# Optimization experiments

Hardware: AMD Instinct MI355X
Metric: run time of the kernel (lower is better)

## Reference

```python
import jax, jax.numpy as jnp
import numpy as np

H, D = 20, 64  # heads, head_dim (hidden_size = 1280)


def setup_inputs() -> dict:
    key = jax.random.key(0)
    ks = jax.random.split(key, 10)
    B, S, HID, CROSS, T_TXT, T_IP = 8, 4096, 1280, 2048, 77, 4
    w = lambda k, shp: jax.random.normal(k, shp, dtype=jnp.float32) * 0.02
    return {
        "hidden_states": jax.random.normal(ks[0], (B, S, HID), dtype=jnp.float32),
        "encoder_hidden_states": jax.random.normal(ks[1], (B, T_TXT, CROSS), dtype=jnp.float32),
        "ip_hidden_states": jax.random.normal(ks[2], (B, T_IP, CROSS), dtype=jnp.float32),
        "Wq": w(ks[3], (HID, HID)),
        "Wk": w(ks[4], (CROSS, HID)),
        "Wv": w(ks[5], (CROSS, HID)),
        "Wk_ip": w(ks[6], (CROSS, HID)),
        "Wv_ip": w(ks[7], (CROSS, HID)),
        "Wo": w(ks[8], (HID, HID)),
        "bo": jnp.zeros((HID,), dtype=jnp.float32),
    }


def _attend(q, kv_in, Wk, Wv):
    # q: [B,S,H,D]; kv_in: [B,T,cross]
    B, T = kv_in.shape[0], kv_in.shape[1]
    k = (kv_in @ Wk).reshape(B, T, H, D)
    v = (kv_in @ Wv).reshape(B, T, H, D)
    scale = 1.0 / jnp.sqrt(jnp.asarray(D, q.dtype))
    scores = jnp.einsum("bqhd,bkhd->bhqk", q, k) * scale
    probs = jax.nn.softmax(scores, axis=-1)
    out = jnp.einsum("bhqk,bkhd->bqhd", probs, v)
    return out.reshape(B, q.shape[1], H * D)


def reference(hidden_states, encoder_hidden_states, ip_hidden_states,
              Wq, Wk, Wv, Wk_ip, Wv_ip, Wo, bo):
    B, S, _ = hidden_states.shape
    q = (hidden_states @ Wq).reshape(B, S, H, D)
    # text cross-attention branch
    out = _attend(q, encoder_hidden_states, Wk, Wv)
    # IP-adapter branch (single adapter, scale=1.0, no mask)
    ip_scale = 1.0
    out = out + ip_scale * _attend(q, ip_hidden_states, Wk_ip, Wv_ip)
    # output projection (dropout is identity at inference)
    return out @ Wo + bo
```

## Files before the change

kernel.cpp:

```cpp
#include <hip/hip_runtime.h>

using u16 = unsigned short;
using u32 = unsigned int;
typedef __bf16 bf16x8 __attribute__((ext_vector_type(8)));
typedef float f32x4 __attribute__((ext_vector_type(4)));
typedef float f32x16 __attribute__((ext_vector_type(16)));

__device__ __forceinline__ u16 f2bf(float f) {
  u32 u = __float_as_uint(f);
  u += 0x7FFFu + ((u >> 16) & 1u);
  return (u16)(u >> 16);
}

__device__ __forceinline__ u32 cvtpk(float a, float b) {
  u32 r;
  asm("v_cvt_pk_bf16_f32 %0, %1, %2" : "=v"(r) : "v"(a), "v"(b));
  return r;
}

__device__ __forceinline__ void gload16(const u16* g, u16* l) {
  __builtin_amdgcn_global_load_lds((const __attribute__((address_space(1))) void*)g,
                                   (__attribute__((address_space(3))) void*)l, 16, 0, 0);
}

__global__ void prep_all(const float* __restrict__ enc, const float* __restrict__ ip,
                         u16* __restrict__ a_all,
                         const float* __restrict__ Wk, const float* __restrict__ Wv,
                         const float* __restrict__ Wkip, const float* __restrict__ Wvip,
                         u16* __restrict__ kvw,
                         const float* __restrict__ Wq, const float* __restrict__ Wo,
                         u16* __restrict__ wq_t, u16* __restrict__ wo_t) {
  const int bid = blockIdx.x;
  const int tid = threadIdx.x;
  if (bid < 1536) {
    const int i = bid * 256 + tid;
    const int row = i >> 9;
    const int c4 = i & 511;
    ushort4 o = {0, 0, 0, 0};
    const float4* src = nullptr;
    if (row < 616) src = (const float4*)enc + (size_t)row * 512 + c4;
    else if (row >= 640 && row < 672) src = (const float4*)ip + (size_t)(row - 640) * 512 + c4;
    if (src) {
      const float4 v = *src;
      o.x = f2bf(v.x); o.y = f2bf(v.y); o.z = f2bf(v.z); o.w = f2bf(v.w);
    }
    ((ushort4*)a_all)[i] = o;
    return;
  }
  __shared__ float tile[32][33];
  const int x = tid & 31, y = tid >> 5;
  const float* in;
  u16* out;
  int K, N, n0, k0;
  if (bid < 11776) {
    const int f = bid - 1536;
    const int z = f / 2560, rem = f % 2560;
    in = (z == 0) ? Wk : (z == 1) ? Wv : (z == 2) ? Wkip : Wvip;
    out = kvw + (size_t)z * 1280 * 2048;
    K = 2048; N = 1280;
    n0 = (rem % 40) << 5; k0 = (rem / 40) << 5;
  } else {
    const int f = bid - 11776;
    const int z = f / 1600, rem = f % 1600;
    in = z ? Wo : Wq;
    out = z ? wo_t : wq_t;
    K = 1280; N = 1280;
    n0 = (rem % 40) << 5; k0 = (rem / 40) << 5;
  }
#pragma unroll
  for (int i = 0; i < 32; i += 8)
    tile[y + i][x] = in[(size_t)(k0 + y + i) * N + n0 + x];
  __syncthreads();
#pragma unroll
  for (int i = 0; i < 32; i += 8)
    out[(size_t)(n0 + y + i) * K + k0 + x] = f2bf(tile[x][y + i]);
}

#define MFMA16(a, b, c) __builtin_amdgcn_mfma_f32_16x16x32_bf16(a, b, c, 0, 0, 0)
#define MFMA32(a, b, c) __builtin_amdgcn_mfma_f32_32x32x16_bf16(a, b, c, 0, 0, 0)

__global__ __launch_bounds__(512, 2) void gemm256kv(
    const u16* __restrict__ A, const u16* __restrict__ Bt, u16* __restrict__ Cb,
    const float* __restrict__ convSrc, u16* __restrict__ convDst,
    int M, int N, int K) {
  const int tid = threadIdx.x;

  if (blockIdx.x >= 60) {
    const float4* src = (const float4*)convSrc;
    ushort4* dst = (ushort4*)convDst;
    const long base = (long)(blockIdx.x - 60) * 4096 + tid;
#pragma unroll
    for (int k = 0; k < 8; ++k) {
      const float4 v = src[base + k * 512];
      ushort4 o;
      o.x = f2bf(v.x); o.y = f2bf(v.y); o.z = f2bf(v.z); o.w = f2bf(v.w);
      dst[base + k * 512] = o;
    }
    return;
  }

  __shared__ __align__(16) u16 smem[65536];
  u16* As = smem;
  u16* Bs = smem + 32768;

  const int w = tid >> 6, lane = tid & 63;
  const int lo = lane & 15, hi = lane >> 4;
  const int wm = w >> 2, wn = w & 3;

  const int nbn = N >> 8;
  const int wg = blockIdx.x;
  const int bm = wg / nbn, bn = wg % nbn;
  const int m0 = bm << 8, n0 = bn << 8;
  const int NT = K >> 6;

  const int sr = lane >> 3;
  const int sc8 = ((lane & 7) ^ sr) << 3;
  const u16* pA[2];
  const u16* pB[2];
#pragma unroll
  for (int i = 0; i < 2; ++i) {
    const int rr = (i * 8 + w) * 8 + sr;
    pA[i] = A + (size_t)(m0 + rr) * K + sc8;
    pB[i] = Bt + (size_t)(n0 + rr) * K + sc8;
  }
  const int ch0 = w * 512, ch1 = (8 + w) * 512;

#define STAGE_A(h, tt)                                                     \
  {                                                                        \
    const int ttc = ((tt) < NT) ? (tt) : (NT - 1);                         \
    u16* d = As + ((((tt)&1) * 2 + (h)) << 13);                            \
    const size_t off = (size_t)(h)*128 * K + (size_t)ttc * 64;             \
    gload16(pA[0] + off, d + ch0);                                         \
    gload16(pA[1] + off, d + ch1);                                         \
  }
#define STAGE_B(h, tt)                                                     \
  {                                                                        \
    const int ttc = ((tt) < NT) ? (tt) : (NT - 1);                         \
    u16* d = Bs + ((((tt)&1) * 2 + (h)) << 13);                            \
    const size_t off = (size_t)(h)*128 * K + (size_t)ttc * 64;             \
    gload16(pB[0] + off, d + ch0);                                         \
    gload16(pB[1] + off, d + ch1);                                         \
  }

  const int low0 = (lo << 7) | ((hi ^ (lo & 7)) << 4);
  const int low1 = (lo << 7) | (((4 | hi) ^ (lo & 7)) << 4);

  f32x4 acc[8][4];
#pragma unroll
  for (int i = 0; i < 8; ++i)
#pragma unroll
    for (int j = 0; j < 4; ++j) acc[i][j] = (f32x4){0.f, 0.f, 0.f, 0.f};

  STAGE_B(0, 0); STAGE_B(1, 0);
  STAGE_A(0, 0); STAGE_A(1, 0);
  STAGE_B(0, 1); STAGE_B(1, 1);

  const char* aSm = (const char*)As;
  const char* bSm = (const char*)Bs;

  for (int t = 0; t < NT; ++t) {
    const int p = t & 1;
    const int aBase = (p * 2 + wm) << 14;
    const int bBase = ((p * 2 + (wn >> 1)) << 14) + ((wn & 1) << 13);

    asm volatile("s_waitcnt vmcnt(4)" ::: "memory");
    asm volatile("s_barrier" ::: "memory");

    bf16x8 a0[4][2], a1[4][2], b0[2][2], b1[2][2];
#pragma unroll
    for (int mf = 0; mf < 4; ++mf) {
      a0[mf][0] = *(const bf16x8*)(aSm + aBase + (mf << 11) + low0);
      a0[mf][1] = *(const bf16x8*)(aSm + aBase + (mf << 11) + low1);
    }
#pragma unroll
    for (int nf = 0; nf < 2; ++nf) {
      b0[nf][0] = *(const bf16x8*)(bSm + bBase + (nf << 11) + low0);
      b0[nf][1] = *(const bf16x8*)(bSm + bBase + (nf << 11) + low1);
    }
    STAGE_A(0, t + 1);
    __builtin_amdgcn_s_setprio(1);
#pragma unroll
    for (int mf = 0; mf < 4; ++mf)
#pragma unroll
      for (int nf = 0; nf < 2; ++nf) {
        acc[mf][nf] = MFMA16(a0[mf][0], b0[nf][0], acc[mf][nf]);
        acc[mf][nf] = MFMA16(a0[mf][1], b0[nf][1], acc[mf][nf]);
      }
    __builtin_amdgcn_s_setprio(0);

#pragma unroll
    for (int nf = 0; nf < 2; ++nf) {
      b1[nf][0] = *(const bf16x8*)(bSm + bBase + (1 << 12) + (nf << 11) + low0);
      b1[nf][1] = *(const bf16x8*)(bSm + bBase + (1 << 12) + (nf << 11) + low1);
    }
    STAGE_A(1, t + 1);
    __builtin_amdgcn_s_setprio(1);
#pragma unroll
    for (int mf = 0; mf < 4; ++mf)
#pragma unroll
      for (int nf = 0; nf < 2; ++nf) {
        acc[mf][2 + nf] = MFMA16(a0[mf][0], b1[nf][0], acc[mf][2 + nf]);
        acc[mf][2 + nf] = MFMA16(a0[mf][1], b1[nf][1], acc[mf][2 + nf]);
      }
    __builtin_amdgcn_s_setprio(0);
    asm volatile("s_barrier" ::: "memory");

#pragma unroll
    for (int mf = 0; mf < 4; ++mf) {
      a1[mf][0] = *(const bf16x8*)(aSm + aBase + (1 << 13) + (mf << 11) + low0);
      a1[mf][1] = *(const bf16x8*)(aSm + aBase + (1 << 13) + (mf << 11) + low1);
    }
    STAGE_B(0, t + 2);
    __builtin_amdgcn_s_setprio(1);
#pragma unroll
    for (int mf = 0; mf < 4; ++mf)
#pragma unroll
      for (int nf = 0; nf < 2; ++nf) {
        acc[4 + mf][nf] = MFMA16(a1[mf][0], b0[nf][0], acc[4 + mf][nf]);
        acc[4 + mf][nf] = MFMA16(a1[mf][1], b0[nf][1], acc[4 + mf][nf]);
      }
    __builtin_amdgcn_s_setprio(0);

    STAGE_B(1, t + 2);
    __builtin_amdgcn_s_setprio(1);
#pragma unroll
    for (int mf = 0; mf < 4; ++mf)
#pragma unroll
      for (int nf = 0; nf < 2; ++nf) {
        acc[4 + mf][2 + nf] = MFMA16(a1[mf][0], b1[nf][0], acc[4 + mf][2 + nf]);
        acc[4 + mf][2 + nf] = MFMA16(a1[mf][1], b1[nf][1], acc[4 + mf][2 + nf]);
      }
    __builtin_amdgcn_s_setprio(0);
  }

#pragma unroll
  for (int g = 0; g < 2; ++g)
#pragma unroll
    for (int mf = 0; mf < 4; ++mf)
#pragma unroll
      for (int ng = 0; ng < 2; ++ng)
#pragma unroll
        for (int nfi = 0; nfi < 2; ++nfi) {
          const f32x4 v = acc[g * 4 + mf][ng * 2 + nfi];
          const int row0 = m0 + wm * 128 + g * 64 + mf * 16 + hi * 4;
          const int col = n0 + wn * 64 + ng * 32 + nfi * 16 + lo;
#pragma unroll
          for (int r = 0; r < 4; ++r)
            Cb[(size_t)(row0 + r) * N + col] = f2bf(v[r]);
        }
#undef STAGE_A
#undef STAGE_B
}

template <int MODE>
__global__ __launch_bounds__(256, 2) void gemm128(
    const u16* __restrict__ A, const u16* __restrict__ Bt,
    u16* __restrict__ Cb, float* __restrict__ Cf, const float* __restrict__ bias,
    const u16* __restrict__ kvcP, const u16* __restrict__ vtP,
    int M, int N, int K) {
  __shared__ __align__(16) u16 smem[32768];
  const int tid = threadIdx.x;
  const int w = tid >> 6, lane = tid & 63;
  const int lo = lane & 15, hi = lane >> 4;
  const int wm = w >> 1, wn = w & 1;

  const int nbn = N >> 7;
  int wg = blockIdx.x;
  {
    const int nwg = gridDim.x;
    const int q = nwg >> 3, r = nwg & 7;
    const int xcd = wg & 7, l = wg >> 3;
    wg = (xcd < r ? xcd * (q + 1) : r * (q + 1) + (xcd - r) * q) + l;
  }
  const int bm = wg / nbn, bn = wg % nbn;
  const int m0 = bm << 7, n0 = bn << 7;
  const int NT = K >> 6;

  const int sr = lane >> 3;
  const int sc8 = ((lane & 7) ^ sr) << 3;
  const u16 *pA[4], *pB[4];
#pragma unroll
  for (int j = 0; j < 4; ++j) {
    const int rr = (w + j * 4) * 8 + sr;
    pA[j] = A + (size_t)(m0 + rr) * K + sc8;
    pB[j] = Bt + (size_t)(n0 + rr) * K + sc8;
  }

#define STG128(tt)                                                         \
  {                                                                        \
    const int ttc = ((tt) < NT) ? (tt) : (NT - 1);                         \
    const int bofs = (((tt)&1) << 13);          \
    const size_t off = (size_t)ttc * 64;                                   \
    _Pragma("unroll") for (int j = 0; j < 4; ++j) {                        \
      gload16(pA[j] + off, smem + bofs + (w + j * 4) * 512);               \
      gload16(pB[j] + off, smem + 16384 + bofs + (w + j * 4) * 512);       \
    }                                                                      \
  }

  const int low0 = (lo << 7) | ((hi ^ (lo & 7)) << 4);
  const int low1 = (lo << 7) | (((4 | hi) ^ (lo & 7)) << 4);
  const char* aSm = (const char*)smem;
  const char* bSm = (const char*)(smem + 16384);

  f32x4 acc[4][4];
#pragma unroll
  for (int i = 0; i < 4; ++i)
#pragma unroll
    for (int j = 0; j < 4; ++j) acc[i][j] = (f32x4){0.f, 0.f, 0.f, 0.f};

  STG128(0); STG128(1);

  for (int t = 0; t < NT; ++t) {
    const int aBase = ((t & 1) << 14) + (wm << 13);
    const int bBase = ((t & 1) << 14) + (wn << 13);

    asm volatile("s_waitcnt vmcnt(8)" ::: "memory");
    asm volatile("s_barrier" ::: "memory");

    bf16x8 a[4][2], b[4][2];
#pragma unroll
    for (int mf = 0; mf < 4; ++mf) {
      a[mf][0] = *(const bf16x8*)(aSm + aBase + (mf << 11) + low0);
      a[mf][1] = *(const bf16x8*)(aSm + aBase + (mf << 11) + low1);
    }
#pragma unroll
    for (int nf = 0; nf < 4; ++nf) {
      b[nf][0] = *(const bf16x8*)(bSm + bBase + (nf << 11) + low0);
      b[nf][1] = *(const bf16x8*)(bSm + bBase + (nf << 11) + low1);
    }
    asm volatile("s_waitcnt lgkmcnt(0)" ::: "memory");
    __builtin_amdgcn_sched_barrier(0);
    asm volatile("s_barrier" ::: "memory");
    STG128(t + 2);
    __builtin_amdgcn_s_setprio(1);
#pragma unroll
    for (int mf = 0; mf < 4; ++mf)
#pragma unroll
      for (int nf = 0; nf < 4; ++nf) {
        acc[mf][nf] = MFMA16(a[mf][0], b[nf][0], acc[mf][nf]);
        acc[mf][nf] = MFMA16(a[mf][1], b[nf][1], acc[mf][nf]);
      }
    __builtin_amdgcn_s_setprio(0);
  }

  if (MODE == 1) {
#pragma unroll
    for (int mf = 0; mf < 4; ++mf)
#pragma unroll
      for (int nf = 0; nf < 4; ++nf) {
        const int row0 = m0 + wm * 64 + mf * 16 + hi * 4;
        const int col = n0 + wn * 64 + nf * 16 + lo;
        const float bb = bias[col];
#pragma unroll
        for (int r = 0; r < 4; ++r)
          Cf[(size_t)(row0 + r) * N + col] = acc[mf][nf][r] + bb;
      }
  } else {
    const int l31 = lane & 31, hi5 = lane >> 5;
    const int h = bn * 2 + wn;
    const int b = m0 >> 12;

    bf16x8 kreg[3][4];
#pragma unroll
    for (int kf = 0; kf < 3; ++kf) {
      const int key = kf * 32 + l31;
      const u16* kp;
      if (key < 77) kp = kvcP + (size_t)(b * 77 + key) * 5120 + h * 64 + hi5 * 8;
      else if (key >= 80 && key < 84)
        kp = kvcP + (size_t)(640 + b * 4 + key - 80) * 5120 + 2560 + h * 64 + hi5 * 8;
      else kp = kvcP + h * 64 + hi5 * 8;
#pragma unroll
      for (int dc = 0; dc < 4; ++dc) kreg[kf][dc] = *(const bf16x8*)(kp + dc * 16);
    }

    asm volatile("s_waitcnt vmcnt(0)" ::: "memory");
    __builtin_amdgcn_s_barrier();

    u16* qlds = smem + w * 4224;
#pragma unroll
    for (int mf = 0; mf < 4; ++mf)
#pragma unroll
      for (int nf = 0; nf < 4; ++nf) {
        const f32x4 v = acc[mf][nf];
        const int qrow = mf * 16 + hi * 4;
        const int d = nf * 16 + lo;
#pragma unroll
        for (int r = 0; r < 4; ++r) qlds[(qrow + r) * 66 + d] = f2bf(v[r]);
      }

    bf16x8 qf0[4], qf1[4];
#pragma unroll
    for (int dc = 0; dc < 4; ++dc) {
      qf0[dc] = *(const bf16x8*)&qlds[(l31)*66 + dc * 16 + hi5 * 8];
      qf1[dc] = *(const bf16x8*)&qlds[(32 + l31) * 66 + dc * 16 + hi5 * 8];
    }

    f32x16 s0[3], s1[3];
#pragma unroll
    for (int kf = 0; kf < 3; ++kf)
#pragma unroll
      for (int r = 0; r < 16; ++r) { s0[kf][r] = 0.f; s1[kf][r] = 0.f; }

#pragma unroll
    for (int kf = 0; kf < 3; ++kf)
#pragma unroll
      for (int dc = 0; dc < 4; ++dc) {
        s0[kf] = MFMA32(kreg[kf][dc], qf0[dc], s0[kf]);
        s1[kf] = MFMA32(kreg[kf][dc], qf1[dc], s1[kf]);
      }

    float st0 = 0.f, si0 = 0.f, st1 = 0.f, si1 = 0.f;
#pragma unroll
    for (int kf = 0; kf < 3; ++kf)
#pragma unroll
      for (int r = 0; r < 16; ++r) {
        const int krem = (r & 3) + 8 * (r >> 2);
        const int k = kf * 32 + krem + 4 * hi5;
        const bool vtx = k < 77;
        const bool vip = (k >= 80) & (k < 84);
        const float e0 = (vtx | vip) ? __expf(s0[kf][r] * 0.125f) : 0.f;
        const float e1 = (vtx | vip) ? __expf(s1[kf][r] * 0.125f) : 0.f;
        s0[kf][r] = e0; s1[kf][r] = e1;
        st0 += vtx ? e0 : 0.f; si0 += vip ? e0 : 0.f;
        st1 += vtx ? e1 : 0.f; si1 += vip ? e1 : 0.f;
      }
    st0 += __shfl_xor(st0, 32); si0 += __shfl_xor(si0, 32);
    st1 += __shfl_xor(st1, 32); si1 += __shfl_xor(si1, 32);
    const float rt0 = __fdividef(1.f, st0), ri0 = __fdividef(1.f, si0);
    const float rt1 = __fdividef(1.f, st1), ri1 = __fdividef(1.f, si1);
#pragma unroll
    for (int kf = 0; kf < 3; ++kf)
#pragma unroll
      for (int r = 0; r < 16; ++r) {
        const int krem = (r & 3) + 8 * (r >> 2);
        const int k = kf * 32 + krem + 4 * hi5;
        const bool vip = (k >= 80) & (k < 84);
        s0[kf][r] *= vip ? ri0 : rt0;
        s1[kf][r] *= vip ? ri1 : rt1;
      }

    const u16* vbase = vtP + ((size_t)(b * 20 + h) * 64) * 96 + hi5 * 8;
    const int rowB = m0 + wm * 64;

#define PV_STORE(sA, qoff)                                                  \
    {                                                                       \
      f32x16 pacc[2];                                                       \
      _Pragma("unroll") for (int nf = 0; nf < 2; ++nf)                      \
      _Pragma("unroll") for (int r = 0; r < 16; ++r) pacc[nf][r] = 0.f;     \
      _Pragma("unroll") for (int ks = 0; ks < 6; ++ks) {                    \
        const int kf = ks >> 1;                                             \
        const int rb = (ks & 1) * 8;                                        \
        const u32 lo01 = cvtpk(sA[kf][rb + 0], sA[kf][rb + 1]);             \
        const u32 lo23 = cvtpk(sA[kf][rb + 2], sA[kf][rb + 3]);             \
        const u32 hi01 = cvtpk(sA[kf][rb + 4], sA[kf][rb + 5]);             \
        const u32 hi23 = cvtpk(sA[kf][rb + 6], sA[kf][rb + 7]);             \
        const u32 plo01 = __shfl_xor(lo01, 32);                             \
        const u32 plo23 = __shfl_xor(lo23, 32);                             \
        const u32 phi01 = __shfl_xor(hi01, 32);                             \
        const u32 phi23 = __shfl_xor(hi23, 32);                             \
        union { u32 u[4]; bf16x8 v; } pu;                                   \
        pu.u[0] = hi5 ? phi01 : lo01;                                       \
        pu.u[1] = hi5 ? phi23 : lo23;                                       \
        pu.u[2] = hi5 ? hi01 : plo01;                                       \
        pu.u[3] = hi5 ? hi23 : plo23;                                       \
        _Pragma("unroll") for (int nf = 0; nf < 2; ++nf) {                  \
          const bf16x8 vb = *(const bf16x8*)(vbase +                        \
              (size_t)(nf * 32 + l31) * 96 + ks * 16);                      \
          pacc[nf] = MFMA32(pu.v, vb, pacc[nf]);                            \
        }                                                                   \
      }                                                                     \
      _Pragma("unroll") for (int nf = 0; nf < 2; ++nf)                      \
      _Pragma("unroll") for (int r = 0; r < 16; ++r) {                      \
        const int row = rowB + (qoff) + (r & 3) + 8 * (r >> 2) + 4 * hi5;   \
        Cb[(size_t)row * 1280 + h * 64 + nf * 32 + l31] = f2bf(pacc[nf][r]);\
      }                                                                     \
    }

    PV_STORE(s0, 0)
    PV_STORE(s1, 32)
#undef PV_STORE
  }
#undef STG128
}

__global__ __launch_bounds__(256) void build_vt(const u16* __restrict__ kvc,
                                                u16* __restrict__ vt) {
  __shared__ u16 Ls[96][72];
  const int tid = threadIdx.x;
  const int h = blockIdx.x % 20, b = blockIdx.x / 20;
  for (int idx = tid; idx < 96 * 8; idx += 256) {
    const int row = idx >> 3, c8 = (idx & 7) << 3;
    uint4 val = make_uint4(0, 0, 0, 0);
    if (row < 77)
      val = *(const uint4*)(kvc + (size_t)(b * 77 + row) * 5120 + 1280 + h * 64 + c8);
    else if (row >= 80 && row < 84)
      val = *(const uint4*)(kvc + (size_t)(640 + b * 4 + row - 80) * 5120 + 3840 + h * 64 + c8);
    *(uint4*)&Ls[row][c8] = val;
  }
  __syncthreads();
  u16* dst = vt + (size_t)blockIdx.x * 64 * 96;
  for (int idx = tid; idx < 768; idx += 256) {
    const int d = idx / 12, c = (idx % 12) * 8;
    u16 tmp[8];
#pragma unroll
    for (int j = 0; j < 8; ++j) tmp[j] = Ls[c + j][d];
    *(uint4*)(dst + d * 96 + c) = *(const uint4*)tmp;
  }
}

extern "C" void kernel_launch(void* const* d_in, const int* in_sizes, int n_in,
                              void* d_out, int out_size, void* d_ws, size_t ws_size,
                              hipStream_t stream) {
  (void)in_sizes; (void)n_in; (void)out_size; (void)ws_size;
  const float* hs   = (const float*)d_in[0];
  const float* enc  = (const float*)d_in[1];
  const float* ip   = (const float*)d_in[2];
  const float* Wq   = (const float*)d_in[3];
  const float* Wk   = (const float*)d_in[4];
  const float* Wv   = (const float*)d_in[5];
  const float* Wkip = (const float*)d_in[6];
  const float* Wvip = (const float*)d_in[7];
  const float* Wo   = (const float*)d_in[8];
  const float* bo   = (const float*)d_in[9];
  float* out = (float*)d_out;

  u16* wq_t  = (u16*)d_out;
  u16* hs_bf = (u16*)d_out + 41943040;

  char* ws = (char*)d_ws;
  u16* kvc   = (u16*)(ws);
  u16* wo_t  = (u16*)(ws + 15728640);
  u16* vt    = (u16*)(ws + 19005440);
  u16* attn  = (u16*)(ws + 20971520);
  u16* kvw   = (u16*)(ws + 20971520 + 3276800);
  u16* a_all = (u16*)(ws + 20971520 + 24248320);

  prep_all<<<14976, 256, 0, stream>>>(enc, ip, a_all, Wk, Wv, Wkip, Wvip, kvw,
                                      Wq, Wo, wq_t, wo_t);

  gemm256kv<<<2620, 512, 0, stream>>>(a_all, kvw, kvc, hs, hs_bf, 768, 5120, 2048);
  build_vt<<<160, 256, 0, stream>>>(kvc, vt);

  gemm128<2><<<2560, 256, 0, stream>>>(hs_bf, wq_t, attn, nullptr, nullptr,
                                       kvc, vt, 32768, 1280, 1280);

  gemm128<1><<<2560, 256, 0, stream>>>(attn, wo_t, nullptr, out, bo,
                                       nullptr, nullptr, 32768, 1280, 1280);
}
```

Measured before the change: 347.3 us.

## Split fused Q-projection attention into separate GEMM and attention kernels

Q projection GEMM now writes bf16 Q to global memory, and a new standalone attn3 kernel computes the text+IP attention from it instead of doing it in the GEMM epilogue. The hidden_states fp32-to-bf16 conversion is moved from the KV GEMM launch into the prep kernel. This frees the GEMM epilogue of the register and LDS pressure of attention, but adds a full write and re-read of Q through HBM plus an extra launch.

```diff
diff --git a/kernel.cpp b/kernel.cpp
--- a/kernel.cpp
+++ b/kernel.cpp
@@ -29,9 +29,23 @@
                          const float* __restrict__ Wkip, const float* __restrict__ Wvip,
                          u16* __restrict__ kvw,
                          const float* __restrict__ Wq, const float* __restrict__ Wo,
-                         u16* __restrict__ wq_t, u16* __restrict__ wo_t) {
+                         u16* __restrict__ wq_t, u16* __restrict__ wo_t,
+                         const float* __restrict__ hs, u16* __restrict__ hs_bf) {
   const int bid = blockIdx.x;
   const int tid = threadIdx.x;
+  if (bid >= 14976) {
+    const float4* src = (const float4*)hs;
+    ushort4* dst = (ushort4*)hs_bf;
+    const long base = (long)(bid - 14976) * 4096 + tid;
+#pragma unroll
+    for (int k = 0; k < 16; ++k) {
+      const float4 v = src[base + k * 256];
+      ushort4 o;
+      o.x = f2bf(v.x); o.y = f2bf(v.y); o.z = f2bf(v.z); o.w = f2bf(v.w);
+      dst[base + k * 256] = o;
+    }
+    return;
+  }
   if (bid < 1536) {
     const int i = bid * 256 + tid;
     const int row = i >> 9;
@@ -81,24 +95,8 @@
 
 __global__ __launch_bounds__(512, 2) void gemm256kv(
     const u16* __restrict__ A, const u16* __restrict__ Bt, u16* __restrict__ Cb,
-    const float* __restrict__ convSrc, u16* __restrict__ convDst,
     int M, int N, int K) {
   const int tid = threadIdx.x;
-
-  if (blockIdx.x >= 60) {
-    const float4* src = (const float4*)convSrc;
-    ushort4* dst = (ushort4*)convDst;
-    const long base = (long)(blockIdx.x - 60) * 4096 + tid;
-#pragma unroll
-    for (int k = 0; k < 8; ++k) {
-      const float4 v = src[base + k * 512];
-      ushort4 o;
-      o.x = f2bf(v.x); o.y = f2bf(v.y); o.z = f2bf(v.z); o.w = f2bf(v.w);
-      dst[base + k * 512] = o;
-    }
-    return;
-  }
-
   __shared__ __align__(16) u16 smem[65536];
   u16* As = smem;
   u16* Bs = smem + 32768;
@@ -256,7 +254,6 @@
 __global__ __launch_bounds__(256, 2) void gemm128(
     const u16* __restrict__ A, const u16* __restrict__ Bt,
     u16* __restrict__ Cb, float* __restrict__ Cf, const float* __restrict__ bias,
-    const u16* __restrict__ kvcP, const u16* __restrict__ vtP,
     int M, int N, int K) {
   __shared__ __align__(16) u16 smem[32768];
   const int tid = threadIdx.x;
@@ -343,144 +340,144 @@
     __builtin_amdgcn_s_setprio(0);
   }
 
-  if (MODE == 1) {
-#pragma unroll
-    for (int mf = 0; mf < 4; ++mf)
-#pragma unroll
-      for (int nf = 0; nf < 4; ++nf) {
-        const int row0 = m0 + wm * 64 + mf * 16 + hi * 4;
-        const int col = n0 + wn * 64 + nf * 16 + lo;
+#pragma unroll
+  for (int mf = 0; mf < 4; ++mf)
+#pragma unroll
+    for (int nf = 0; nf < 4; ++nf) {
+      const int row0 = m0 + wm * 64 + mf * 16 + hi * 4;
+      const int col = n0 + wn * 64 + nf * 16 + lo;
+      if (MODE == 1) {
         const float bb = bias[col];
 #pragma unroll
         for (int r = 0; r < 4; ++r)
           Cf[(size_t)(row0 + r) * N + col] = acc[mf][nf][r] + bb;
+      } else {
+#pragma unroll
+        for (int r = 0; r < 4; ++r)
+          Cb[(size_t)(row0 + r) * N + col] = f2bf(acc[mf][nf][r]);
       }
-  } else {
-    const int l31 = lane & 31, hi5 = lane >> 5;
-    const int h = bn * 2 + wn;
-    const int b = m0 >> 12;
-
-    bf16x8 kreg[3][4];
-#pragma unroll
-    for (int kf = 0; kf < 3; ++kf) {
-      const int key = kf * 32 + l31;
-      const u16* kp;
-      if (key < 77) kp = kvcP + (size_t)(b * 77 + key) * 5120 + h * 64 + hi5 * 8;
-      else if (key >= 80 && key < 84)
-        kp = kvcP + (size_t)(640 + b * 4 + key - 80) * 5120 + 2560 + h * 64 + hi5 * 8;
-      else kp = kvcP + h * 64 + hi5 * 8;
-#pragma unroll
-      for (int dc = 0; dc < 4; ++dc) kreg[kf][dc] = *(const bf16x8*)(kp + dc * 16);
-    }
-
-    asm volatile("s_waitcnt vmcnt(0)" ::: "memory");
-    __builtin_amdgcn_s_barrier();
-
-    u16* qlds = smem + w * 4224;
-#pragma unroll
-    for (int mf = 0; mf < 4; ++mf)
-#pragma unroll
-      for (int nf = 0; nf < 4; ++nf) {
-        const f32x4 v = acc[mf][nf];
-        const int qrow = mf * 16 + hi * 4;
-        const int d = nf * 16 + lo;
-#pragma unroll
-        for (int r = 0; r < 4; ++r) qlds[(qrow + r) * 66 + d] = f2bf(v[r]);
-      }
-
-    bf16x8 qf0[4], qf1[4];
+    }
+#undef STG128
+}
+
+__global__ __launch_bounds__(256) void attn3(
+    const u16* __restrict__ Q, const u16* __restrict__ kvc,
+    const u16* __restrict__ vt, u16* __restrict__ O) {
+  const int tid = threadIdx.x;
+  const int w = tid >> 6, lane = tid & 63;
+  const int l31 = lane & 31, hi5 = lane >> 5;
+  const int bid = blockIdx.x;
+  const int qc = bid & 15;
+  const int h = (bid >> 4) % 20;
+  const int b = bid / 320;
+  const int q0 = qc * 256 + w * 64;
+  const size_t qbase = (size_t)b * 4096 + q0;
+
+  bf16x8 qf0[4], qf1[4];
+  {
+    const u16* qp0 = Q + (qbase + l31) * 1280 + h * 64 + hi5 * 8;
+    const u16* qp1 = Q + (qbase + 32 + l31) * 1280 + h * 64 + hi5 * 8;
 #pragma unroll
     for (int dc = 0; dc < 4; ++dc) {
-      qf0[dc] = *(const bf16x8*)&qlds[(l31)*66 + dc * 16 + hi5 * 8];
-      qf1[dc] = *(const bf16x8*)&qlds[(32 + l31) * 66 + dc * 16 + hi5 * 8];
-    }
-
-    f32x16 s0[3], s1[3];
-#pragma unroll
-    for (int kf = 0; kf < 3; ++kf)
-#pragma unroll
-      for (int r = 0; r < 16; ++r) { s0[kf][r] = 0.f; s1[kf][r] = 0.f; }
-
-#pragma unroll
-    for (int kf = 0; kf < 3; ++kf)
-#pragma unroll
-      for (int dc = 0; dc < 4; ++dc) {
-        s0[kf] = MFMA32(kreg[kf][dc], qf0[dc], s0[kf]);
-        s1[kf] = MFMA32(kreg[kf][dc], qf1[dc], s1[kf]);
-      }
-
-    float st0 = 0.f, si0 = 0.f, st1 = 0.f, si1 = 0.f;
-#pragma unroll
-    for (int kf = 0; kf < 3; ++kf)
-#pragma unroll
-      for (int r = 0; r < 16; ++r) {
-        const int krem = (r & 3) + 8 * (r >> 2);
-        const int k = kf * 32 + krem + 4 * hi5;
-        const bool vtx = k < 77;
-        const bool vip = (k >= 80) & (k < 84);
-        const float e0 = (vtx | vip) ? __expf(s0[kf][r] * 0.125f) : 0.f;
-        const float e1 = (vtx | vip) ? __expf(s1[kf][r] * 0.125f) : 0.f;
-        s0[kf][r] = e0; s1[kf][r] = e1;
-        st0 += vtx ? e0 : 0.f; si0 += vip ? e0 : 0.f;
-        st1 += vtx ? e1 : 0.f; si1 += vip ? e1 : 0.f;
-      }
-    st0 += __shfl_xor(st0, 32); si0 += __shfl_xor(si0, 32);
-    st1 += __shfl_xor(st1, 32); si1 += __shfl_xor(si1, 32);
-    const float rt0 = __fdividef(1.f, st0), ri0 = __fdividef(1.f, si0);
-    const float rt1 = __fdividef(1.f, st1), ri1 = __fdividef(1.f, si1);
-#pragma unroll
-    for (int kf = 0; kf < 3; ++kf)
-#pragma unroll
-      for (int r = 0; r < 16; ++r) {
-        const int krem = (r & 3) + 8 * (r >> 2);
-        const int k = kf * 32 + krem + 4 * hi5;
-        const bool vip = (k >= 80) & (k < 84);
-        s0[kf][r] *= vip ? ri0 : rt0;
-        s1[kf][r] *= vip ? ri1 : rt1;
-      }
-
-    const u16* vbase = vtP + ((size_t)(b * 20 + h) * 64) * 96 + hi5 * 8;
-    const int rowB = m0 + wm * 64;
+      qf0[dc] = *(const bf16x8*)(qp0 + dc * 16);
+      qf1[dc] = *(const bf16x8*)(qp1 + dc * 16);
+    }
+  }
+
+  f32x16 s0[3], s1[3];
+#pragma unroll
+  for (int kf = 0; kf < 3; ++kf)
+#pragma unroll
+    for (int r = 0; r < 16; ++r) { s0[kf][r] = 0.f; s1[kf][r] = 0.f; }
+
+#pragma unroll
+  for (int kf = 0; kf < 3; ++kf) {
+    const int key = kf * 32 + l31;
+    const u16* kp;
+    if (key < 77) kp = kvc + (size_t)(b * 77 + key) * 5120 + h * 64 + hi5 * 8;
+    else if (key >= 80 && key < 84)
+      kp = kvc + (size_t)(640 + b * 4 + key - 80) * 5120 + 2560 + h * 64 + hi5 * 8;
+    else kp = kvc + h * 64 + hi5 * 8;
+    bf16x8 ka[4];
+#pragma unroll
+    for (int dc = 0; dc < 4; ++dc) ka[dc] = *(const bf16x8*)(kp + dc * 16);
+#pragma unroll
+    for (int dc = 0; dc < 4; ++dc) {
+      s0[kf] = MFMA32(ka[dc], qf0[dc], s0[kf]);
+      s1[kf] = MFMA32(ka[dc], qf1[dc], s1[kf]);
+    }
+  }
+
+  float st0 = 0.f, si0 = 0.f, st1 = 0.f, si1 = 0.f;
+#pragma unroll
+  for (int kf = 0; kf < 3; ++kf)
+#pragma unroll
+    for (int r = 0; r < 16; ++r) {
+      const int krem = (r & 3) + 8 * (r >> 2);
+      const int k = kf * 32 + krem + 4 * hi5;
+      const bool vtx = k < 77;
+      const bool vip = (k >= 80) & (k < 84);
+      const float e0 = (vtx | vip) ? __expf(s0[kf][r] * 0.125f) : 0.f;
+      const float e1 = (vtx | vip) ? __expf(s1[kf][r] * 0.125f) : 0.f;
+      s0[kf][r] = e0; s1[kf][r] = e1;
+      st0 += vtx ? e0 : 0.f; si0 += vip ? e0 : 0.f;
+      st1 += vtx ? e1 : 0.f; si1 += vip ? e1 : 0.f;
+    }
+  st0 += __shfl_xor(st0, 32); si0 += __shfl_xor(si0, 32);
+  st1 += __shfl_xor(st1, 32); si1 += __shfl_xor(si1, 32);
+  const float rt0 = __fdividef(1.f, st0), ri0 = __fdividef(1.f, si0);
+  const float rt1 = __fdividef(1.f, st1), ri1 = __fdividef(1.f, si1);
+#pragma unroll
+  for (int kf = 0; kf < 3; ++kf)
+#pragma unroll
+    for (int r = 0; r < 16; ++r) {
+      const int krem = (r & 3) + 8 * (r >> 2);
+      const int k = kf * 32 + krem + 4 * hi5;
+      const bool vip = (k >= 80) & (k < 84);
+      s0[kf][r] *= vip ? ri0 : rt0;
+      s1[kf][r] *= vip ? ri1 : rt1;
+    }
+
+  const u16* vbase = vt + ((size_t)(b * 20 + h) * 64) * 96 + hi5 * 8;
 
 #define PV_STORE(sA, qoff)                                                  \
-    {                                                                       \
-      f32x16 pacc[2];                                                       \
-      _Pragma("unroll") for (int nf = 0; nf < 2; ++nf)                      \
-      _Pragma("unroll") for (int r = 0; r < 16; ++r) pacc[nf][r] = 0.f;     \
-      _Pragma("unroll") for (int ks = 0; ks < 6; ++ks) {                    \
-        const int kf = ks >> 1;                                             \
-        const int rb = (ks & 1) * 8;                                        \
-        const u32 lo01 = cvtpk(sA[kf][rb + 0], sA[kf][rb + 1]);             \
-        const u32 lo23 = cvtpk(sA[kf][rb + 2], sA[kf][rb + 3]);             \
-        const u32 hi01 = cvtpk(sA[kf][rb + 4], sA[kf][rb + 5]);             \
-        const u32 hi23 = cvtpk(sA[kf][rb + 6], sA[kf][rb + 7]);             \
-        const u32 plo01 = __shfl_xor(lo01, 32);                             \
-        const u32 plo23 = __shfl_xor(lo23, 32);                             \
-        const u32 phi01 = __shfl_xor(hi01, 32);                             \
-        const u32 phi23 = __shfl_xor(hi23, 32);                             \
-        union { u32 u[4]; bf16x8 v; } pu;                                   \
-        pu.u[0] = hi5 ? phi01 : lo01;                                       \
-        pu.u[1] = hi5 ? phi23 : lo23;                                       \
-        pu.u[2] = hi5 ? hi01 : plo01;                                       \
-        pu.u[3] = hi5 ? hi23 : plo23;                                       \
-        _Pragma("unroll") for (int nf = 0; nf < 2; ++nf) {                  \
-          const bf16x8 vb = *(const bf16x8*)(vbase +                        \
-              (size_t)(nf * 32 + l31) * 96 + ks * 16);                      \
-          pacc[nf] = MFMA32(pu.v, vb, pacc[nf]);                            \
-        }                                                                   \
+  {                                                                         \
+    f32x16 acc[2];                                                          \
+    _Pragma("unroll") for (int nf = 0; nf < 2; ++nf)                        \
+    _Pragma("unroll") for (int r = 0; r < 16; ++r) acc[nf][r] = 0.f;        \
+    _Pragma("unroll") for (int ks = 0; ks < 6; ++ks) {                      \
+      const int kf = ks >> 1;                                               \
+      const int rb = (ks & 1) * 8;                                          \
+      const u32 lo01 = cvtpk(sA[kf][rb + 0], sA[kf][rb + 1]);               \
+      const u32 lo23 = cvtpk(sA[kf][rb + 2], sA[kf][rb + 3]);               \
+      const u32 hi01 = cvtpk(sA[kf][rb + 4], sA[kf][rb + 5]);               \
+      const u32 hi23 = cvtpk(sA[kf][rb + 6], sA[kf][rb + 7]);               \
+      const u32 plo01 = __shfl_xor(lo01, 32);                               \
+      const u32 plo23 = __shfl_xor(lo23, 32);                               \
+      const u32 phi01 = __shfl_xor(hi01, 32);                               \
+      const u32 phi23 = __shfl_xor(hi23, 32);                               \
+      union { u32 u[4]; bf16x8 v; } pu;                                     \
+      pu.u[0] = hi5 ? phi01 : lo01;                                         \
+      pu.u[1] = hi5 ? phi23 : lo23;                                         \
+      pu.u[2] = hi5 ? hi01 : plo01;                                         \
+      pu.u[3] = hi5 ? hi23 : plo23;                                         \
+      _Pragma("unroll") for (int nf = 0; nf < 2; ++nf) {                    \
+        const bf16x8 vb =                                                   \
+            *(const bf16x8*)(vbase + (size_t)(nf * 32 + l31) * 96 + ks * 16);\
+        acc[nf] = MFMA32(pu.v, vb, acc[nf]);                                \
       }                                                                     \
-      _Pragma("unroll") for (int nf = 0; nf < 2; ++nf)                      \
-      _Pragma("unroll") for (int r = 0; r < 16; ++r) {                      \
-        const int row = rowB + (qoff) + (r & 3) + 8 * (r >> 2) + 4 * hi5;   \
-        Cb[(size_t)row * 1280 + h * 64 + nf * 32 + l31] = f2bf(pacc[nf][r]);\
-      }                                                                     \
-    }
-
-    PV_STORE(s0, 0)
-    PV_STORE(s1, 32)
+    }                                                                       \
+    _Pragma("unroll") for (int nf = 0; nf < 2; ++nf)                        \
+    _Pragma("unroll") for (int r = 0; r < 16; ++r) {                        \
+      const int row = q0 + (qoff) + (r & 3) + 8 * (r >> 2) + 4 * hi5;       \
+      O[((size_t)b * 4096 + row) * 1280 + h * 64 + nf * 32 + l31] =         \
+          f2bf(acc[nf][r]);                                                 \
+    }                                                                       \
+  }
+
+  PV_STORE(s0, 0)
+  PV_STORE(s1, 32)
 #undef PV_STORE
-  }
-#undef STG128
 }
 
 __global__ __launch_bounds__(256) void build_vt(const u16* __restrict__ kvc,
@@ -524,26 +521,29 @@
   const float* bo   = (const float*)d_in[9];
   float* out = (float*)d_out;
 
-  u16* wq_t  = (u16*)d_out;
-  u16* hs_bf = (u16*)d_out + 41943040;
+  u16* hs_bf = (u16*)d_out;
+  u16* q_bf  = (u16*)d_out + 41943040;
 
   char* ws = (char*)d_ws;
   u16* kvc   = (u16*)(ws);
   u16* wo_t  = (u16*)(ws + 15728640);
   u16* vt    = (u16*)(ws + 19005440);
   u16* attn  = (u16*)(ws + 20971520);
+  u16* wq_t  = attn;
   u16* kvw   = (u16*)(ws + 20971520 + 3276800);
   u16* a_all = (u16*)(ws + 20971520 + 24248320);
 
-  prep_all<<<14976, 256, 0, stream>>>(enc, ip, a_all, Wk, Wv, Wkip, Wvip, kvw,
-                                      Wq, Wo, wq_t, wo_t);
-
-  gemm256kv<<<2620, 512, 0, stream>>>(a_all, kvw, kvc, hs, hs_bf, 768, 5120, 2048);
+  prep_all<<<17536, 256, 0, stream>>>(enc, ip, a_all, Wk, Wv, Wkip, Wvip, kvw,
+                                      Wq, Wo, wq_t, wo_t, hs, hs_bf);
+
+  gemm256kv<<<60, 512, 0, stream>>>(a_all, kvw, kvc, 768, 5120, 2048);
   build_vt<<<160, 256, 0, stream>>>(kvc, vt);
 
-  gemm128<2><<<2560, 256, 0, stream>>>(hs_bf, wq_t, attn, nullptr, nullptr,
-                                       kvc, vt, 32768, 1280, 1280);
+  gemm128<0><<<2560, 256, 0, stream>>>(hs_bf, wq_t, q_bf, nullptr, nullptr,
+                                       32768, 1280, 1280);
+
+  attn3<<<2560, 256, 0, stream>>>(q_bf, kvc, vt, attn);
 
   gemm128<1><<<2560, 256, 0, stream>>>(attn, wo_t, nullptr, out, bo,
-                                       nullptr, nullptr, 32768, 1280, 1280);
-}
+                                       32768, 1280, 1280);
+}
```

New measurement: 408.6 us. 1.18x slower.
